# Optimization experiments

Hardware: AMD Instinct MI355X
Metric: run time of the kernel (lower is better)

## Reference

```python
import jax, jax.numpy as jnp
import numpy as np

EPS = 1e-6
BETA = 0.25
NVQ_W = 1.0


def _mlp(h, params):
    # Linear + ReLU on all but last layer (dropout=0, bn=False)
    n = len(params)
    for i, (w, b) in enumerate(params):
        h = h @ w + b
        if i < n - 1:
            h = jax.nn.relu(h)
    return h


def _kuma_ab(a_raw, b_raw):
    return jax.nn.softplus(a_raw) + EPS, jax.nn.softplus(b_raw) + EPS


def _kuma_h(z, a, b):
    x = jnp.clip(jax.nn.sigmoid(z), EPS, 1.0 - EPS)
    inner = jnp.clip(1.0 - x ** a, EPS, 1.0)
    y = 1.0 - inner ** b
    return jnp.clip(y, EPS, 1.0 - EPS)


def _kuma_h_inv(y, a, b):
    y = jnp.clip(y, EPS, 1.0 - EPS)
    omy = jnp.clip(1.0 - y, EPS, 1.0)
    inner = jnp.clip(1.0 - omy ** (1.0 / b), EPS, 1.0 - EPS)
    x = jnp.clip(inner ** (1.0 / a), EPS, 1.0 - EPS)
    return jnp.log(x / (1.0 - x))


def _rq(z, codebooks):
    # Residual VQ: per level, squared-L2 nearest code (argmin), straight-through,
    # codebook + beta*commitment loss. sk_epsilon=0 -> Sinkhorn skipped.
    sg = jax.lax.stop_gradient
    residual = z
    x_q = jnp.zeros_like(z)
    losses, idx_list = [], []
    for l in range(codebooks.shape[0]):
        cb = codebooks[l]  # [K, D]
        d = (jnp.sum(residual * residual, -1, keepdims=True)
             + jnp.sum(cb * cb, -1)
             - 2.0 * residual @ cb.T)  # [B, K]
        idx = jnp.argmin(d, axis=-1)  # [B]
        q = cb[idx]  # [B, D]
        codebook_loss = jnp.mean((q - sg(residual)) ** 2)
        commit_loss = jnp.mean((sg(q) - residual) ** 2)
        losses.append(codebook_loss + BETA * commit_loss)
        q_st = residual + sg(q - residual)  # straight-through
        residual = residual - q_st
        x_q = x_q + q_st
        idx_list.append(idx)
    return x_q, jnp.mean(jnp.stack(losses)), jnp.stack(idx_list, axis=-1)


def _forward(x, enc, dec, codebooks, a_raw, b_raw):
    z = _mlp(x, enc)
    a, b = _kuma_ab(a_raw, b_raw)
    z_prime = _kuma_h(z, a, b)
    zq_prime, rq_loss, indices = _rq(z_prime, codebooks)
    z_q = _kuma_h_inv(zq_prime, a, b)
    z_recon = _kuma_h_inv(z_prime, a, b)
    nvq_loss = jnp.mean((z_recon - z) ** 2)
    total_quant_loss = rq_loss + NVQ_W * nvq_loss
    out = _mlp(z_q, dec)
    return out, total_quant_loss, indices


def setup_inputs() -> dict:
    key = jax.random.key(0)
    ks = jax.random.split(key, 16)
    B, IN = 16384, 768
    enc_dims = [768, 2048, 1024, 512, 128]
    dec_dims = enc_dims[::-1]

    def lin(k, din, dout):
        w = jax.random.normal(k, (din, dout), jnp.float32) * (1.0 / np.sqrt(din))
        return w, jnp.zeros((dout,), jnp.float32)

    inp = {"x": jax.random.normal(ks[0], (B, IN), jnp.float32)}
    for i in range(4):
        w, b = lin(ks[1 + i], enc_dims[i], enc_dims[i + 1])
        inp[f"enc_w{i}"], inp[f"enc_b{i}"] = w, b
        w, b = lin(ks[5 + i], dec_dims[i], dec_dims[i + 1])
        inp[f"dec_w{i}"], inp[f"dec_b{i}"] = w, b
    inp["codebooks"] = jax.random.normal(ks[9], (4, 256, 128), jnp.float32)
    inp["a_raw"] = jnp.zeros((128,), jnp.float32)
    inp["b_raw"] = jnp.zeros((128,), jnp.float32)
    return inp


def reference(x, enc_w0, enc_b0, enc_w1, enc_b1, enc_w2, enc_b2, enc_w3, enc_b3,
              dec_w0, dec_b0, dec_w1, dec_b1, dec_w2, dec_b2, dec_w3, dec_b3,
              codebooks, a_raw, b_raw):
    enc = [(enc_w0, enc_b0), (enc_w1, enc_b1), (enc_w2, enc_b2), (enc_w3, enc_b3)]
    dec = [(dec_w0, dec_b0), (dec_w1, dec_b1), (dec_w2, dec_b2), (dec_w3, dec_b3)]
    return _forward(x, enc, dec, codebooks, a_raw, b_raw)
```

## Files before the change

kernel.cpp:

```cpp
#include <hip/hip_runtime.h>
#include <math.h>

#define EPS_F 1e-6f
#define ONE_M_EPS (1.0f - 1e-6f)

typedef __attribute__((ext_vector_type(8))) short s16x8;
typedef __attribute__((ext_vector_type(8))) _Float16 f16x8;
typedef __attribute__((ext_vector_type(4))) float f32x4;

__device__ __forceinline__ ushort f2bf(float f) {
    union { float f; unsigned u; } v; v.f = f;
    unsigned u = v.u;
    return (ushort)((u + 0x7FFFu + ((u >> 16) & 1u)) >> 16);
}
__device__ __forceinline__ float bf2f(ushort h) {
    union { unsigned u; float f; } v; v.u = ((unsigned)h) << 16;
    return v.f;
}
__device__ __forceinline__ void split2h(float x, ushort& h, ushort& m) {
    union { _Float16 f; ushort u; } a, b;
    a.f = (_Float16)x;
    float r = x - (float)a.f;
    b.f = (_Float16)r;
    h = a.u; m = b.u;
}

#define GLL16(srcp, dstp)                                                     \
    __builtin_amdgcn_global_load_lds(                                         \
        (const __attribute__((address_space(1))) void*)(srcp),                \
        (__attribute__((address_space(3))) void*)(dstp), 16, 0, 0)

__device__ __forceinline__ int swz_k(int row, int k) { return k ^ ((row >> 1) & 3); }

__device__ __forceinline__ void tile_remap(int MB, int NB, int& bm_i, int& bn_i) {
    const int lin = blockIdx.y * MB + blockIdx.x;
    const int nwg = MB * NB;
    int wg = lin;
    if ((nwg & 7) == 0)
        wg = (lin & 7) * (nwg >> 3) + (lin >> 3);
    if (((MB | NB) & 1) == 0) {
        const int tiles_m = MB >> 1;
        const int stile = wg >> 2, within = wg & 3;
        const int st_m = stile % tiles_m, st_n = stile / tiles_m;
        bm_i = st_m * 2 + (within & 1);
        bn_i = st_n * 2 + (within >> 1);
    } else {
        bm_i = wg % MB;
        bn_i = wg / MB;
    }
}

template<bool RELU, int OUT2>
__global__ __launch_bounds__(256) void gemm_mfma_split2(
    const ushort* __restrict__ Ah, const ushort* __restrict__ Am,
    const ushort* __restrict__ Wh, const ushort* __restrict__ Wm,
    const float* __restrict__ bias,
    void* __restrict__ C0, void* __restrict__ C1,
    int M, int N, int K)
{
    __shared__ __align__(16) ushort As[2][2][128 * 32];
    __shared__ __align__(16) ushort Bs[2][2][128 * 32];

    const int tid  = threadIdx.x;
    const int lane = tid & 63;
    const int w    = tid >> 6;
    const int wm   = (w >> 1) * 64;
    const int wn   = (w & 1) * 64;
    int bmi, bni;
    tile_remap(gridDim.x, gridDim.y, bmi, bni);
    const int bm   = bmi * 128;
    const int bn   = bni * 128;

    f32x4 acc[4][4];
#pragma unroll
    for (int i = 0; i < 4; i++)
#pragma unroll
        for (int j = 0; j < 4; j++) acc[i][j] = f32x4{0.f, 0.f, 0.f, 0.f};

    const int c0 = (w * 2) * 64 + lane;
    const int c1 = (w * 2 + 1) * 64 + lane;
    const int r0 = c0 >> 2, k0e = swz_k(r0, c0 & 3) * 8;
    const int r1 = c1 >> 2, k1e = swz_k(r1, c1 & 3) * 8;

    const size_t a_off0 = (size_t)(bm + r0) * K + k0e;
    const size_t a_off1 = (size_t)(bm + r1) * K + k1e;
    const size_t b_off0 = (size_t)(bn + r0) * K + k0e;
    const size_t b_off1 = (size_t)(bn + r1) * K + k1e;
    const int d0 = (w * 2) * 512;
    const int d1 = d0 + 512;

    const ushort* Ap[2] = {Ah, Am};
    const ushort* Wp[2] = {Wh, Wm};

    const int fm  = lane & 15;
    const int fkb = lane >> 4;
    const int NT  = K >> 5;

#pragma unroll
    for (int p = 0; p < 2; p++) {
        GLL16(Ap[p] + a_off0, &As[0][p][d0]);
        GLL16(Ap[p] + a_off1, &As[0][p][d1]);
        GLL16(Wp[p] + b_off0, &Bs[0][p][d0]);
        GLL16(Wp[p] + b_off1, &Bs[0][p][d1]);
    }

    int cur = 0;
    for (int kt = 0; kt < NT; kt++) {
        if (kt + 1 < NT) {
            const int kk = (kt + 1) << 5;
#pragma unroll
            for (int p = 0; p < 2; p++) {
                GLL16(Ap[p] + a_off0 + kk, &As[cur ^ 1][p][d0]);
                GLL16(Ap[p] + a_off1 + kk, &As[cur ^ 1][p][d1]);
                GLL16(Wp[p] + b_off0 + kk, &Bs[cur ^ 1][p][d0]);
                GLL16(Wp[p] + b_off1 + kk, &Bs[cur ^ 1][p][d1]);
            }
            asm volatile("s_waitcnt vmcnt(8)" ::: "memory");
        } else {
            asm volatile("s_waitcnt vmcnt(0)" ::: "memory");
        }
        __builtin_amdgcn_s_barrier();
        asm volatile("" ::: "memory");

        f16x8 af[2][4];
#pragma unroll
        for (int p = 0; p < 2; p++)
#pragma unroll
            for (int i = 0; i < 4; i++) {
                const int row = wm + i * 16 + fm;
                af[p][i] = *reinterpret_cast<const f16x8*>(
                    &As[cur][p][row * 32 + swz_k(row, fkb) * 8]);
            }
        f16x8 bf0[4], bf1[4];
#pragma unroll
        for (int j = 0; j < 4; j++) {
            const int row = wn + j * 16 + fm;
            bf0[j] = *reinterpret_cast<const f16x8*>(&Bs[cur][0][row * 32 + swz_k(row, fkb) * 8]);
            bf1[j] = *reinterpret_cast<const f16x8*>(&Bs[cur][1][row * 32 + swz_k(row, fkb) * 8]);
        }

        __builtin_amdgcn_s_setprio(1);
#pragma unroll
        for (int i = 0; i < 4; i++)
#pragma unroll
            for (int j = 0; j < 4; j++) {
                acc[i][j] = __builtin_amdgcn_mfma_f32_16x16x32_f16(af[0][i], bf0[j], acc[i][j], 0, 0, 0);
                acc[i][j] = __builtin_amdgcn_mfma_f32_16x16x32_f16(af[0][i], bf1[j], acc[i][j], 0, 0, 0);
                acc[i][j] = __builtin_amdgcn_mfma_f32_16x16x32_f16(af[1][i], bf0[j], acc[i][j], 0, 0, 0);
            }
        __builtin_amdgcn_s_setprio(0);
        asm volatile("" ::: "memory");
        __builtin_amdgcn_s_barrier();
        cur ^= 1;
    }

#pragma unroll
    for (int j = 0; j < 4; j++) {
        const int coln = bn + wn + j * 16 + fm;
        const float bv = bias[coln];
#pragma unroll
        for (int i = 0; i < 4; i++) {
            const int row0 = bm + wm + i * 16 + (lane >> 4) * 4;
#pragma unroll
            for (int r = 0; r < 4; r++) {
                float o = acc[i][j][r] + bv;
                if (RELU) o = fmaxf(o, 0.f);
                const size_t idx = (size_t)(row0 + r) * N + coln;
                if (OUT2) {
                    ushort h, m;
                    split2h(o, h, m);
                    ((ushort*)C0)[idx] = h;
                    ((ushort*)C1)[idx] = m;
                } else {
                    ((float*)C0)[idx] = o;
                }
            }
        }
    }
}

template<bool RELU, bool OUT_BF16>
__global__ __launch_bounds__(256) void gemm_mfma_bt(
    const ushort* __restrict__ A, const ushort* __restrict__ WT,
    const float* __restrict__ bias, void* __restrict__ Cv,
    int M, int N, int K)
{
    __shared__ __align__(16) ushort As[2][128 * 32];
    __shared__ __align__(16) ushort Bs[2][128 * 32];

    const int tid  = threadIdx.x;
    const int lane = tid & 63;
    const int w    = tid >> 6;
    const int wm   = (w >> 1) * 64;
    const int wn   = (w & 1) * 64;
    int bmi, bni;
    tile_remap(gridDim.x, gridDim.y, bmi, bni);
    const int bm   = bmi * 128;
    const int bn   = bni * 128;

    f32x4 acc[4][4];
#pragma unroll
    for (int i = 0; i < 4; i++)
#pragma unroll
        for (int j = 0; j < 4; j++) acc[i][j] = f32x4{0.f, 0.f, 0.f, 0.f};

    const int c0 = (w * 2) * 64 + lane;
    const int c1 = (w * 2 + 1) * 64 + lane;
    const int r0 = c0 >> 2, k0e = swz_k(r0, c0 & 3) * 8;
    const int r1 = c1 >> 2, k1e = swz_k(r1, c1 & 3) * 8;

    const ushort* a_src0 = A  + (size_t)(bm + r0) * K + k0e;
    const ushort* a_src1 = A  + (size_t)(bm + r1) * K + k1e;
    const ushort* b_src0 = WT + (size_t)(bn + r0) * K + k0e;
    const ushort* b_src1 = WT + (size_t)(bn + r1) * K + k1e;
    const int d0 = (w * 2) * 512;
    const int d1 = d0 + 512;

    const int fm  = lane & 15;
    const int fkb = lane >> 4;
    const int NT  = K >> 5;

    GLL16(a_src0, &As[0][d0]);
    GLL16(a_src1, &As[0][d1]);
    GLL16(b_src0, &Bs[0][d0]);
    GLL16(b_src1, &Bs[0][d1]);

    int cur = 0;
    for (int kt = 0; kt < NT; kt++) {
        if (kt + 1 < NT) {
            const int kk = (kt + 1) << 5;
            GLL16(a_src0 + kk, &As[cur ^ 1][d0]);
            GLL16(a_src1 + kk, &As[cur ^ 1][d1]);
            GLL16(b_src0 + kk, &Bs[cur ^ 1][d0]);
            GLL16(b_src1 + kk, &Bs[cur ^ 1][d1]);
            asm volatile("s_waitcnt vmcnt(4)" ::: "memory");
        } else {
            asm volatile("s_waitcnt vmcnt(0)" ::: "memory");
        }
        __builtin_amdgcn_s_barrier();
        asm volatile("" ::: "memory");

        s16x8 af[4], bfr[4];
#pragma unroll
        for (int i = 0; i < 4; i++) {
            const int row = wm + i * 16 + fm;
            af[i] = *reinterpret_cast<const s16x8*>(&As[cur][row * 32 + swz_k(row, fkb) * 8]);
        }
#pragma unroll
        for (int j = 0; j < 4; j++) {
            const int row = wn + j * 16 + fm;
            bfr[j] = *reinterpret_cast<const s16x8*>(&Bs[cur][row * 32 + swz_k(row, fkb) * 8]);
        }

        __builtin_amdgcn_s_setprio(1);
#pragma unroll
        for (int i = 0; i < 4; i++)
#pragma unroll
            for (int j = 0; j < 4; j++)
                acc[i][j] = __builtin_amdgcn_mfma_f32_16x16x32_bf16(
                    af[i], bfr[j], acc[i][j], 0, 0, 0);
        __builtin_amdgcn_s_setprio(0);
        asm volatile("" ::: "memory");
        __builtin_amdgcn_s_barrier();
        cur ^= 1;
    }

#pragma unroll
    for (int j = 0; j < 4; j++) {
        const int coln = bn + wn + j * 16 + fm;
        const float bv = bias[coln];
#pragma unroll
        for (int i = 0; i < 4; i++) {
            const int row0 = bm + wm + i * 16 + (lane >> 4) * 4;
#pragma unroll
            for (int r = 0; r < 4; r++) {
                float o = acc[i][j][r] + bv;
                if (RELU) o = fmaxf(o, 0.f);
                if (OUT_BF16)
                    ((ushort*)Cv)[(size_t)(row0 + r) * N + coln] = f2bf(o);
                else
                    ((float*)Cv)[(size_t)(row0 + r) * N + coln] = o;
            }
        }
    }
}

__global__ __launch_bounds__(256) void transpose_to_bf16(
    const float* __restrict__ W, ushort* __restrict__ WT, int K, int N)
{
    __shared__ float t[32][33];
    const int kb = blockIdx.x * 32, nb = blockIdx.y * 32;
    const int tx = threadIdx.x & 31, ty = threadIdx.x >> 5;
#pragma unroll
    for (int i = ty; i < 32; i += 8)
        t[i][tx] = W[(size_t)(kb + i) * N + nb + tx];
    __syncthreads();
#pragma unroll
    for (int i = ty; i < 32; i += 8)
        WT[(size_t)(nb + i) * K + kb + tx] = f2bf(t[tx][i]);
}

__global__ __launch_bounds__(256) void transpose_split_f16(
    const float* __restrict__ W, ushort* __restrict__ TH,
    ushort* __restrict__ TM, int K, int N)
{
    __shared__ float t[32][33];
    const int kb = blockIdx.x * 32, nb = blockIdx.y * 32;
    const int tx = threadIdx.x & 31, ty = threadIdx.x >> 5;
#pragma unroll
    for (int i = ty; i < 32; i += 8)
        t[i][tx] = W[(size_t)(kb + i) * N + nb + tx];
    __syncthreads();
#pragma unroll
    for (int i = ty; i < 32; i += 8) {
        ushort h, m;
        split2h(t[tx][i], h, m);
        const size_t idx = (size_t)(nb + i) * K + kb + tx;
        TH[idx] = h; TM[idx] = m;
    }
}

__global__ __launch_bounds__(256) void split_plane2_kernel(
    const float* __restrict__ X, ushort* __restrict__ H,
    ushort* __restrict__ M, size_t n)
{
    size_t i = (size_t)blockIdx.x * 256 + threadIdx.x;
    if (i >= n) return;
    ushort h, m;
    split2h(X[i], h, m);
    H[i] = h; M[i] = m;
}

__global__ __launch_bounds__(128) void prep_cb_kernel(
    const float* __restrict__ cb, float* __restrict__ cbT, float* __restrict__ cnorm)
{
    int b = blockIdx.x;
    int d = threadIdx.x;
    float v = cb[(size_t)b * 128 + d];
    int l = b >> 8, c = b & 255;
    cbT[((size_t)l * 128 + d) * 256 + c] = v;
    float s = v * v;
#pragma unroll
    for (int off = 32; off > 0; off >>= 1) s += __shfl_down(s, off);
    __shared__ float ps[2];
    if ((d & 63) == 0) ps[d >> 6] = s;
    __syncthreads();
    if (d == 0) cnorm[b] = ps[0] + ps[1];
}

__device__ __forceinline__ float softplusf(float x) {
    return (x > 20.f) ? x : log1pf(expf(x));
}

__global__ void kuma_ab_init(const float* __restrict__ a_raw, const float* __restrict__ b_raw,
                             float* __restrict__ kp)
{
    int t = threadIdx.x;
    if (t < 128) {
        float a = softplusf(a_raw[t]) + EPS_F;
        float b = softplusf(b_raw[t]) + EPS_F;
        kp[t] = a;
        kp[128 + t] = b;
        kp[256 + t] = 1.f / a;
        kp[384 + t] = 1.f / b;
    }
}

__global__ __launch_bounds__(256) void kuma_h_kernel(
    const float* __restrict__ z, const float* __restrict__ kp,
    float* __restrict__ zp, int n)
{
    int i = blockIdx.x * 256 + threadIdx.x;
    if (i >= n) return;
    int col = i & 127;
    float a = kp[col], b = kp[128 + col];
    float zv = z[i];
    float x = 1.f / (1.f + expf(-zv));
    x = fminf(fmaxf(x, EPS_F), ONE_M_EPS);
    float inner = 1.f - powf(x, a);
    inner = fminf(fmaxf(inner, EPS_F), 1.f);
    float y = 1.f - powf(inner, b);
    y = fminf(fmaxf(y, EPS_F), ONE_M_EPS);
    zp[i] = y;
}

__global__ __launch_bounds__(64) void rq_kernel3(
    const float* __restrict__ zp, const float* __restrict__ cb,
    const float* __restrict__ cbT, const float* __restrict__ cnorm,
    float* __restrict__ xq, float* __restrict__ idx_out,
    float* __restrict__ prq, int bid0, int nRq)
{
    __shared__ float res[8][128];

    const int t = threadIdx.x;
    const int row0 = blockIdx.x * 8;

#pragma unroll
    for (int j = 0; j < 16; j++) {
        int e = t + j * 64;
        res[e >> 7][e & 127] = zp[(size_t)row0 * 128 + e];
    }

    float lsum[4];
    int bidx[8];

#pragma unroll 1
    for (int l = 0; l < 4; l++) {
        const float* cT = cbT + (size_t)l * 32768;

        float acc[8][4];
#pragma unroll
        for (int r = 0; r < 8; r++)
#pragma unroll
            for (int cc = 0; cc < 4; cc++) acc[r][cc] = 0.f;

        float pc[16];
#pragma unroll
        for (int dd = 0; dd < 4; dd++)
#pragma unroll
            for (int cc = 0; cc < 4; cc++)
                pc[dd * 4 + cc] = cT[dd * 256 + cc * 64 + t];

#pragma unroll 2
        for (int d = 0; d < 128; d += 4) {
            float nc[16];
            if (d < 124) {
#pragma unroll
                for (int dd = 0; dd < 4; dd++)
#pragma unroll
                    for (int cc = 0; cc < 4; cc++)
                        nc[dd * 4 + cc] = cT[(d + 4 + dd) * 256 + cc * 64 + t];
            }
#pragma unroll
            for (int r = 0; r < 8; r++) {
                float4 rv = *reinterpret_cast<const float4*>(&res[r][d]);
#pragma unroll
                for (int cc = 0; cc < 4; cc++) {
                    acc[r][cc] += rv.x * pc[cc] + rv.y * pc[4 + cc]
                                + rv.z * pc[8 + cc] + rv.w * pc[12 + cc];
                }
            }
#pragma unroll
            for (int k = 0; k < 16; k++) pc[k] = nc[k];
        }

        float cn[4];
#pragma unroll
        for (int cc = 0; cc < 4; cc++) cn[cc] = cnorm[l * 256 + cc * 64 + t];

#pragma unroll
        for (int r = 0; r < 8; r++) {
            float dmin = cn[0] - 2.f * acc[r][0];
            int imin = t;
#pragma unroll
            for (int cc = 1; cc < 4; cc++) {
                float dv = cn[cc] - 2.f * acc[r][cc];
                if (dv < dmin) { dmin = dv; imin = cc * 64 + t; }
            }
#pragma unroll
            for (int off = 1; off < 64; off <<= 1) {
                float d2 = __shfl_xor(dmin, off);
                int i2 = __shfl_xor(imin, off);
                if (d2 < dmin || (d2 == dmin && i2 < imin)) { dmin = d2; imin = i2; }
            }
            bidx[r] = imin;
            if (t == 0) idx_out[(size_t)(row0 + r) * 4 + l] = (float)imin;
        }

        float s = 0.f;
#pragma unroll
        for (int j = 0; j < 16; j++) {
            const int r = j >> 1;
            const int d = (j & 1) * 64 + t;
            float q = cb[((size_t)(l * 256) + bidx[r]) * 128 + d];
            float nr = res[r][d] - q;
            res[r][d] = nr;
            s += nr * nr;
        }
        lsum[l] = s;
    }

#pragma unroll
    for (int j = 0; j < 16; j++) {
        int e = t + j * 64;
        xq[(size_t)row0 * 128 + e] = zp[(size_t)row0 * 128 + e] - res[e >> 7][e & 127];
    }

#pragma unroll
    for (int l = 0; l < 4; l++) {
        float s = lsum[l];
#pragma unroll
        for (int off = 32; off > 0; off >>= 1) s += __shfl_down(s, off);
        if (t == 0) prq[(size_t)l * nRq + bid0 + blockIdx.x] = s;
    }
}

__device__ __forceinline__ float kuma_h_inv_f(float y, float ia, float ib) {
    y = fminf(fmaxf(y, EPS_F), ONE_M_EPS);
    float omy = fminf(fmaxf(1.f - y, EPS_F), 1.f);
    float inner = fminf(fmaxf(1.f - powf(omy, ib), EPS_F), ONE_M_EPS);
    float x = fminf(fmaxf(powf(inner, ia), EPS_F), ONE_M_EPS);
    return logf(x / (1.f - x));
}

__global__ __launch_bounds__(256) void zq_nvq_kernel(
    const float* __restrict__ xq, const float* __restrict__ zp,
    const float* __restrict__ z, const float* __restrict__ kp,
    float* __restrict__ zq, ushort* __restrict__ zq16,
    float* __restrict__ pnvq, int bid0, int n)
{
    int i = blockIdx.x * 256 + threadIdx.x;
    float ds = 0.f;
    if (i < n) {
        int col = i & 127;
        float ia = kp[256 + col], ib = kp[384 + col];
        float xv = xq[i];
        float zpv = zp[i];
        float zv = z[i];
        float zr = kuma_h_inv_f(zpv, ia, ib);
        float d = zr - zv;
        ds = d * d;
        float zqv = kuma_h_inv_f(xv, ia, ib);
        zq[i] = zqv;
        zq16[i] = f2bf(zqv);
    }
#pragma unroll
    for (int off = 32; off > 0; off >>= 1) ds += __shfl_down(ds, off);
    __shared__ float ps[4];
    if ((threadIdx.x & 63) == 0) ps[threadIdx.x >> 6] = ds;
    __syncthreads();
    if (threadIdx.x == 0)
        pnvq[bid0 + blockIdx.x] = ps[0] + ps[1] + ps[2] + ps[3];
}

__global__ __launch_bounds__(256) void finalize_kernel(
    const float* __restrict__ prq, const float* __restrict__ pnvq,
    int nRqAll, int nNvq, float* __restrict__ out_loss)
{
    const int t = threadIdx.x;
    float srq = 0.f, snvq = 0.f;
    for (int i = t; i < nRqAll; i += 256) srq += prq[i];
    for (int i = t; i < nNvq; i += 256) snvq += pnvq[i];
#pragma unroll
    for (int off = 32; off > 0; off >>= 1) {
        srq += __shfl_down(srq, off);
        snvq += __shfl_down(snvq, off);
    }
    __shared__ float pr[4], pn[4];
    if ((t & 63) == 0) { pr[t >> 6] = srq; pn[t >> 6] = snvq; }
    __syncthreads();
    if (t == 0) {
        const float inv = 1.f / (16384.f * 128.f);
        float rq = (pr[0] + pr[1] + pr[2] + pr[3]);
        float nv = (pn[0] + pn[1] + pn[2] + pn[3]);
        out_loss[0] = 0.3125f * rq * inv + nv * inv;
    }
}

extern "C" void kernel_launch(void* const* d_in, const int* in_sizes, int n_in,
                              void* d_out, int out_size, void* d_ws, size_t ws_size,
                              hipStream_t stream)
{
    constexpr int B = 16384;

    const float* x = (const float*)d_in[0];
    const float* enc_w[4]; const float* enc_b[4];
    const float* dec_w[4]; const float* dec_b[4];
    for (int i = 0; i < 4; i++) {
        enc_w[i] = (const float*)d_in[1 + 4 * i];
        enc_b[i] = (const float*)d_in[2 + 4 * i];
        dec_w[i] = (const float*)d_in[3 + 4 * i];
        dec_b[i] = (const float*)d_in[4 + 4 * i];
    }
    const float* cb    = (const float*)d_in[17];
    const float* a_raw = (const float*)d_in[18];
    const float* b_raw = (const float*)d_in[19];

    size_t avail = ws_size / 4;
    const size_t fixed_f = 6547008;
    int R = 16384;
    while (R > 256 && (size_t)R * 3520 + fixed_f > avail) R >>= 1;

    float* ws    = (float*)d_ws;
    float* slotA = ws;
    float* slotB = slotA + (size_t)R * 1024;
    float* zb    = slotB + (size_t)R * 2048;
    float* zpb   = zb  + (size_t)R * 128;
    float* xqb   = zpb + (size_t)R * 128;
    float* zq16f = xqb + (size_t)R * 128;
    float* fixp  = zq16f + (size_t)R * 64;

    ushort* ew = (ushort*)fixp;
    ushort* e0h = ew;            ushort* e0m = e0h + 1572864;
    ushort* e1h = e0m + 1572864; ushort* e1m = e1h + 2097152;
    ushort* e2h = e1m + 2097152; ushort* e2m = e2h + 524288;
    ushort* e3h = e2m + 524288;  ushort* e3m = e3h + 65536;
    ushort* wt0 = e3m + 65536;
    ushort* wt1 = wt0 + 65536;
    ushort* wt2 = wt1 + 524288;
    ushort* wt3 = wt2 + 2097152;
    float* cbT   = (float*)(wt3 + 1572864);
    float* cnorm = cbT + 4 * 128 * 256;
    float* kp    = cnorm + 4 * 256;
    float* prq   = kp + 512;
    float* pnvq  = prq + 16384;

    ushort* zq16 = (ushort*)zq16f;

    ushort* xH  = (ushort*)slotA;  ushort* xM  = xH  + (size_t)R * 768;
    ushort* h0H = (ushort*)slotB;  ushort* h0M = h0H + (size_t)R * 2048;
    ushort* h1H = (ushort*)slotA;  ushort* h1M = h1H + (size_t)R * 1024;
    ushort* h2H = (ushort*)slotB;  ushort* h2M = h2H + (size_t)R * 512;

    ushort* dA = (ushort*)slotB;
    ushort* dB = (ushort*)(slotB + (size_t)R * 256);
    ushort* dC = (ushort*)slotA;

    float* out      = (float*)d_out;
    float* out_loss = out + (size_t)B * 768;
    float* out_idx  = out_loss + 1;

    prep_cb_kernel<<<1024, 128, 0, stream>>>(cb, cbT, cnorm);
    kuma_ab_init<<<1, 128, 0, stream>>>(a_raw, b_raw, kp);
    transpose_split_f16<<<dim3( 768/32, 2048/32), 256, 0, stream>>>(enc_w[0], e0h, e0m,  768, 2048);
    transpose_split_f16<<<dim3(2048/32, 1024/32), 256, 0, stream>>>(enc_w[1], e1h, e1m, 2048, 1024);
    transpose_split_f16<<<dim3(1024/32,  512/32), 256, 0, stream>>>(enc_w[2], e2h, e2m, 1024,  512);
    transpose_split_f16<<<dim3( 512/32,  128/32), 256, 0, stream>>>(enc_w[3], e3h, e3m,  512,  128);
    transpose_to_bf16<<<dim3(128/32,  512/32), 256, 0, stream>>>(dec_w[0], wt0,  128,  512);
    transpose_to_bf16<<<dim3(512/32, 1024/32), 256, 0, stream>>>(dec_w[1], wt1,  512, 1024);
    transpose_to_bf16<<<dim3(1024/32,2048/32), 256, 0, stream>>>(dec_w[2], wt2, 1024, 2048);
    transpose_to_bf16<<<dim3(2048/32, 768/32), 256, 0, stream>>>(dec_w[3], wt3, 2048,  768);

    const int nc = B / R;
    const int nRq = B / 8;
    const int rqPerChunk = R / 8;
    const int nvqPerChunk = (R * 128) / 256;
    for (int c = 0; c < nc; c++) {
        const size_t base = (size_t)c * R;
        const float* xc = x + base * 768;
        float* outc = out + base * 768;
        float* idxc = out_idx + base * 4;

        {
            size_t n = (size_t)R * 768;
            split_plane2_kernel<<<(unsigned)((n + 255) / 256), 256, 0, stream>>>(xc, xH, xM, n);
        }

        gemm_mfma_split2<true , 1><<<dim3(R/128, 16), 256, 0, stream>>>(
            xH, xM, e0h, e0m, enc_b[0], h0H, h0M, R, 2048, 768);
        gemm_mfma_split2<true , 1><<<dim3(R/128,  8), 256, 0, stream>>>(
            h0H, h0M, e1h, e1m, enc_b[1], h1H, h1M, R, 1024, 2048);
        gemm_mfma_split2<true , 1><<<dim3(R/128,  4), 256, 0, stream>>>(
            h1H, h1M, e2h, e2m, enc_b[2], h2H, h2M, R,  512, 1024);
        gemm_mfma_split2<false, 0><<<dim3(R/128,  1), 256, 0, stream>>>(
            h2H, h2M, e3h, e3m, enc_b[3], zb, nullptr, R, 128, 512);

        kuma_h_kernel<<<(R * 128) / 256, 256, 0, stream>>>(zb, kp, zpb, R * 128);
        rq_kernel3<<<rqPerChunk, 64, 0, stream>>>(zpb, cb, cbT, cnorm, xqb, idxc,
                                                  prq, c * rqPerChunk, nRq);
        zq_nvq_kernel<<<nvqPerChunk, 256, 0, stream>>>(xqb, zpb, zb, kp, xqb, zq16,
                                                       pnvq, c * nvqPerChunk, R * 128);

        gemm_mfma_bt<true , true ><<<dim3(R/128,  4), 256, 0, stream>>>(zq16, wt0, dec_b[0], dA, R,  512,  128);
        gemm_mfma_bt<true , true ><<<dim3(R/128,  8), 256, 0, stream>>>(dA,   wt1, dec_b[1], dB, R, 1024,  512);
        gemm_mfma_bt<true , true ><<<dim3(R/128, 16), 256, 0, stream>>>(dB,   wt2, dec_b[2], dC, R, 2048, 1024);
        gemm_mfma_bt<false, false><<<dim3(R/128,  6), 256, 0, stream>>>(dC,   wt3, dec_b[3], outc, R,  768, 2048);
    }

    finalize_kernel<<<1, 256, 0, stream>>>(prq, pnvq, 4 * nRq, B * 128 / 256, out_loss);
}
```

Before: 874.9 us.

## Widen RQ row tile, vectorize input split, use fast math in inverse Kumaraswamy

The residual-quantization kernel now handles 16 rows per block instead of 8, so each codebook element loaded from memory is reused across twice as many rows and the block count is halved. The fp16 split kernel for the input now reads float4 and writes packed 64-bit stores. The inverse Kumaraswamy transform swaps powf/logf for __expf/__logf intrinsics. The larger RQ tile raises register pressure and cuts parallelism, and the fast intrinsics may lose accuracy near the clamps.

Measured after the change: 882.3 us. Within noise of the previous version (+0.8%).

```diff
diff --git a/kernel.cpp b/kernel.cpp
--- a/kernel.cpp
+++ b/kernel.cpp
@@ -320,15 +320,20 @@
     }
 }
 
-__global__ __launch_bounds__(256) void split_plane2_kernel(
-    const float* __restrict__ X, ushort* __restrict__ H,
-    ushort* __restrict__ M, size_t n)
+__global__ __launch_bounds__(256) void split_plane2v_kernel(
+    const float4* __restrict__ X, ushort* __restrict__ H,
+    ushort* __restrict__ M, size_t n4)
 {
     size_t i = (size_t)blockIdx.x * 256 + threadIdx.x;
-    if (i >= n) return;
-    ushort h, m;
-    split2h(X[i], h, m);
-    H[i] = h; M[i] = m;
+    if (i >= n4) return;
+    float4 v = X[i];
+    union { ushort u[4]; unsigned long long ll; } h, m;
+    split2h(v.x, h.u[0], m.u[0]);
+    split2h(v.y, h.u[1], m.u[1]);
+    split2h(v.z, h.u[2], m.u[2]);
+    split2h(v.w, h.u[3], m.u[3]);
+    *reinterpret_cast<unsigned long long*>(&H[i * 4]) = h.ll;
+    *reinterpret_cast<unsigned long long*>(&M[i * 4]) = m.ll;
 }
 
 __global__ __launch_bounds__(128) void prep_cb_kernel(
@@ -384,33 +389,33 @@
     zp[i] = y;
 }
 
-__global__ __launch_bounds__(64) void rq_kernel3(
+__global__ __launch_bounds__(64) void rq_kernel4(
     const float* __restrict__ zp, const float* __restrict__ cb,
     const float* __restrict__ cbT, const float* __restrict__ cnorm,
     float* __restrict__ xq, float* __restrict__ idx_out,
     float* __restrict__ prq, int bid0, int nRq)
 {
-    __shared__ float res[8][128];
+    __shared__ float res[16][128];
 
     const int t = threadIdx.x;
-    const int row0 = blockIdx.x * 8;
-
-#pragma unroll
-    for (int j = 0; j < 16; j++) {
+    const int row0 = blockIdx.x * 16;
+
+#pragma unroll
+    for (int j = 0; j < 32; j++) {
         int e = t + j * 64;
         res[e >> 7][e & 127] = zp[(size_t)row0 * 128 + e];
     }
 
     float lsum[4];
-    int bidx[8];
+    int bidx[16];
 
 #pragma unroll 1
     for (int l = 0; l < 4; l++) {
         const float* cT = cbT + (size_t)l * 32768;
 
-        float acc[8][4];
-#pragma unroll
-        for (int r = 0; r < 8; r++)
+        float acc[16][4];
+#pragma unroll
+        for (int r = 0; r < 16; r++)
 #pragma unroll
             for (int cc = 0; cc < 4; cc++) acc[r][cc] = 0.f;
 
@@ -432,7 +437,7 @@
                         nc[dd * 4 + cc] = cT[(d + 4 + dd) * 256 + cc * 64 + t];
             }
 #pragma unroll
-            for (int r = 0; r < 8; r++) {
+            for (int r = 0; r < 16; r++) {
                 float4 rv = *reinterpret_cast<const float4*>(&res[r][d]);
 #pragma unroll
                 for (int cc = 0; cc < 4; cc++) {
@@ -449,7 +454,7 @@
         for (int cc = 0; cc < 4; cc++) cn[cc] = cnorm[l * 256 + cc * 64 + t];
 
 #pragma unroll
-        for (int r = 0; r < 8; r++) {
+        for (int r = 0; r < 16; r++) {
             float dmin = cn[0] - 2.f * acc[r][0];
             int imin = t;
 #pragma unroll
@@ -469,7 +474,7 @@
 
         float s = 0.f;
 #pragma unroll
-        for (int j = 0; j < 16; j++) {
+        for (int j = 0; j < 32; j++) {
             const int r = j >> 1;
             const int d = (j & 1) * 64 + t;
             float q = cb[((size_t)(l * 256) + bidx[r]) * 128 + d];
@@ -481,7 +486,7 @@
     }
 
 #pragma unroll
-    for (int j = 0; j < 16; j++) {
+    for (int j = 0; j < 32; j++) {
         int e = t + j * 64;
         xq[(size_t)row0 * 128 + e] = zp[(size_t)row0 * 128 + e] - res[e >> 7][e & 127];
     }
@@ -495,6 +500,14 @@
     }
 }
 
+__device__ __forceinline__ float kuma_h_inv_fast(float y, float ia, float ib) {
+    y = fminf(fmaxf(y, EPS_F), ONE_M_EPS);
+    float omy = fminf(fmaxf(1.f - y, EPS_F), 1.f);
+    float p1 = __expf(ib * __logf(omy));
+    float inner = fminf(fmaxf(1.f - p1, EPS_F), ONE_M_EPS);
+    float x = fminf(fmaxf(__expf(ia * __logf(inner)), EPS_F), ONE_M_EPS);
+    return __logf(x / (1.f - x));
+}
 __device__ __forceinline__ float kuma_h_inv_f(float y, float ia, float ib) {
     y = fminf(fmaxf(y, EPS_F), ONE_M_EPS);
     float omy = fminf(fmaxf(1.f - y, EPS_F), 1.f);
@@ -517,10 +530,10 @@
         float xv = xq[i];
         float zpv = zp[i];
         float zv = z[i];
-        float zr = kuma_h_inv_f(zpv, ia, ib);
+        float zr = kuma_h_inv_fast(zpv, ia, ib);
         float d = zr - zv;
         ds = d * d;
-        float zqv = kuma_h_inv_f(xv, ia, ib);
+        float zqv = kuma_h_inv_fast(xv, ia, ib);
         zq[i] = zqv;
         zq16[i] = f2bf(zqv);
     }
@@ -632,8 +645,8 @@
     transpose_to_bf16<<<dim3(2048/32, 768/32), 256, 0, stream>>>(dec_w[3], wt3, 2048,  768);
 
     const int nc = B / R;
-    const int nRq = B / 8;
-    const int rqPerChunk = R / 8;
+    const int nRq = B / 16;
+    const int rqPerChunk = R / 16;
     const int nvqPerChunk = (R * 128) / 256;
     for (int c = 0; c < nc; c++) {
         const size_t base = (size_t)c * R;
@@ -642,8 +655,9 @@
         float* idxc = out_idx + base * 4;
 
         {
-            size_t n = (size_t)R * 768;
-            split_plane2_kernel<<<(unsigned)((n + 255) / 256), 256, 0, stream>>>(xc, xH, xM, n);
+            size_t n4 = (size_t)R * 768 / 4;
+            split_plane2v_kernel<<<(unsigned)((n4 + 255) / 256), 256, 0, stream>>>(
+                (const float4*)xc, xH, xM, n4);
         }
 
         gemm_mfma_split2<true , 1><<<dim3(R/128, 16), 256, 0, stream>>>(
@@ -656,7 +670,7 @@
             h2H, h2M, e3h, e3m, enc_b[3], zb, nullptr, R, 128, 512);
 
         kuma_h_kernel<<<(R * 128) / 256, 256, 0, stream>>>(zb, kp, zpb, R * 128);
-        rq_kernel3<<<rqPerChunk, 64, 0, stream>>>(zpb, cb, cbT, cnorm, xqb, idxc,
+        rq_kernel4<<<rqPerChunk, 64, 0, stream>>>(zpb, cb, cbT, cnorm, xqb, idxc,
                                                   prq, c * rqPerChunk, nRq);
         zq_nvq_kernel<<<nvqPerChunk, 256, 0, stream>>>(xqb, zpb, zb, kp, xqb, zq16,
                                                        pnvq, c * nvqPerChunk, R * 128);
```
